# Kernel optimization log

Hardware: AMD Instinct MI355X
Metric: run time of the kernel (lower is better)

Reference implementation:

```python
import jax, jax.numpy as jnp
import numpy as np

DIM = 768
NUM_HEADS = 12
HEAD_DIM = DIM // NUM_HEADS


def setup_inputs() -> dict:
    key = jax.random.key(0)
    k1, k2, k3 = jax.random.split(key, 3)
    B, N, C = 1, 4096, DIM
    x = jax.random.normal(k1, (B, N, C), dtype=jnp.float32)
    w_qkv = jax.random.normal(k2, (C, 3 * C), dtype=jnp.float32) * (C ** -0.5)
    w_proj = jax.random.normal(k3, (C, C), dtype=jnp.float32) * (C ** -0.5)
    b_proj = jnp.zeros((C,), dtype=jnp.float32)
    return {"x": x, "w_qkv": w_qkv, "w_proj": w_proj, "b_proj": b_proj}


def reference(x, w_qkv, w_proj, b_proj):
    B, N, C = x.shape
    H, D = NUM_HEADS, HEAD_DIM
    scale = D ** -0.5
    # QKV projection (no bias), split into heads: [B, N, 3, H, D] -> bhnd
    qkv = (x @ w_qkv).reshape(B, N, 3, H, D)
    qkv = jnp.transpose(qkv, (2, 0, 3, 1, 4))  # [3, B, H, N, D]
    q, k, v = qkv[0], qkv[1], qkv[2]
    # world_size == 1 => all_gather is identity; full attention over N
    attn = jnp.einsum('bhnd,bhmd->bhnm', q * scale, k)
    attn = jax.nn.softmax(attn, axis=-1)
    out = jnp.einsum('bhnm,bhmd->bhnd', attn, v)
    out = jnp.transpose(out, (0, 2, 1, 3)).reshape(B, N, C)
    return out @ w_proj + b_proj
```

## Files before the change

kernel.cpp:

```cpp
#include <hip/hip_runtime.h>
#include <hip/hip_bf16.h>

#define NT 4096
#define CD 768
#define NH 12
#define HD 64
#define CQ 2304

typedef __bf16 bf;
typedef __bf16 v8bf __attribute__((ext_vector_type(8)));
typedef __bf16 v4bf __attribute__((ext_vector_type(4)));
typedef float  v4f  __attribute__((ext_vector_type(4)));

__device__ __forceinline__ void gld16(const bf* g, bf* l) {
  __builtin_amdgcn_global_load_lds(
      (__attribute__((address_space(1))) void*)g,
      (__attribute__((address_space(3))) void*)l,
      16, 0, 0);
}

__device__ __forceinline__ float fexp2(float x) {
#if defined(__HIP_DEVICE_COMPILE__)
  return __builtin_amdgcn_exp2f(x);
#else
  return x;
#endif
}

__global__ __launch_bounds__(256) void prep(
    const float* __restrict__ x, const float* __restrict__ wqkv,
    const float* __restrict__ wproj, bf* __restrict__ Xb,
    bf* __restrict__ WqkvT, bf* __restrict__ WpT) {
  __shared__ float tile[32][33];
  const int b = blockIdx.x, tid = threadIdx.x;
  if (b < 3072) {
    const int i = b * 256 + tid;
    const float4 v = ((const float4*)x)[i];
    bf o4[4] = {(bf)v.x, (bf)v.y, (bf)v.z, (bf)v.w};
    ((ushort4*)Xb)[i] = *(const ushort4*)o4;
    return;
  }
  const float* in;
  bf* out;
  int rows, cols, c0, r0;
  if (b < 4800) {
    const int t = b - 3072;
    in = wqkv; out = WqkvT; rows = CD; cols = CQ;
    c0 = (t % 72) * 32; r0 = (t / 72) * 32;
  } else {
    const int t = b - 4800;
    in = wproj; out = WpT; rows = CD; cols = CD;
    c0 = (t % 24) * 32; r0 = (t / 24) * 32;
  }
  const int tx = tid & 31, ty = tid >> 5;
#pragma unroll
  for (int j = 0; j < 32; j += 8)
    tile[ty + j][tx] = in[(size_t)(r0 + ty + j) * cols + (c0 + tx)];
  __syncthreads();
#pragma unroll
  for (int j = 0; j < 32; j += 8)
    out[(size_t)(c0 + ty + j) * rows + (r0 + tx)] = (bf)tile[tx][ty + j];
}

__global__ __launch_bounds__(256, 3) void gemm_qkv(
    const bf* __restrict__ A, const bf* __restrict__ Bt,
    bf* __restrict__ Qb, bf* __restrict__ Kb, bf* __restrict__ Vtb) {
  __shared__ __align__(16) bf As[128 * 64];
  __shared__ __align__(16) bf Bs[128 * 64];
  const int tid = threadIdx.x;
  const int lane = tid & 63, wave = tid >> 6;
  const int lane15 = lane & 15, quad = lane >> 4;
  const int waveM = wave & 1, waveN = wave >> 1;
  const int bm = blockIdx.x * 128;
  const int bn = blockIdx.y * 128;

  v4f acc[4][4];
#pragma unroll
  for (int i = 0; i < 4; ++i)
#pragma unroll
    for (int j = 0; j < 4; ++j) acc[i][j] = (v4f){0.f, 0.f, 0.f, 0.f};

  for (int k0 = 0; k0 < CD; k0 += 64) {
#pragma unroll
    for (int p = 0; p < 4; ++p) {
      const int t = tid + p * 256;
      const int r = t >> 3, u = t & 7;
      gld16(A + (size_t)(bm + r) * CD + k0 + ((u ^ (r & 7)) << 3), As + t * 8);
    }
#pragma unroll
    for (int p = 0; p < 4; ++p) {
      const int t = tid + p * 256;
      const int r = t >> 3, u = t & 7;
      gld16(Bt + (size_t)(bn + r) * CD + k0 + ((u ^ (r & 7)) << 3), Bs + t * 8);
    }
    asm volatile("s_waitcnt vmcnt(0)" ::: "memory");
    __syncthreads();

    v8bf af[4][2], bfr[4][2];
#pragma unroll
    for (int mt = 0; mt < 4; ++mt) {
      const int rr = waveM * 64 + mt * 16 + lane15;
      const int r7 = rr & 7;
      af[mt][0] = *(const v8bf*)(As + rr * 64 + ((quad ^ r7) << 3));
      af[mt][1] = *(const v8bf*)(As + rr * 64 + (((quad ^ 4) ^ r7) << 3));
    }
#pragma unroll
    for (int nt = 0; nt < 4; ++nt) {
      const int rr = waveN * 64 + nt * 16 + lane15;
      const int r7 = rr & 7;
      bfr[nt][0] = *(const v8bf*)(Bs + rr * 64 + ((quad ^ r7) << 3));
      bfr[nt][1] = *(const v8bf*)(Bs + rr * 64 + (((quad ^ 4) ^ r7) << 3));
    }
#pragma unroll
    for (int mt = 0; mt < 4; ++mt)
#pragma unroll
      for (int nt = 0; nt < 4; ++nt) {
        acc[mt][nt] = __builtin_amdgcn_mfma_f32_16x16x32_bf16(af[mt][0], bfr[nt][0], acc[mt][nt], 0, 0, 0);
        acc[mt][nt] = __builtin_amdgcn_mfma_f32_16x16x32_bf16(af[mt][1], bfr[nt][1], acc[mt][nt], 0, 0, 0);
      }
    __syncthreads();
  }

  const float QSCALE = 0.125f * 1.4426950408889634f;
#pragma unroll
  for (int mt = 0; mt < 4; ++mt) {
    const int rowB = bm + waveM * 64 + mt * 16 + quad * 4;
#pragma unroll
    for (int nt = 0; nt < 4; ++nt) {
      const int col = bn + waveN * 64 + nt * 16 + lane15;
      const int s = col / CD;
      const int rem = col - s * CD;
      const int h = rem >> 6, d = rem & 63;
      if (s == 2) {
        bf vp[4];
#pragma unroll
        for (int i = 0; i < 4; ++i) vp[i] = (bf)acc[mt][nt][i];
        const int pos = (rowB & ~31) + (((rowB & 15) >> 2) << 3) + (((rowB >> 4) & 1) << 2);
        *(uint2*)(Vtb + ((size_t)h * HD + d) * NT + pos) = *(const uint2*)vp;
      } else {
#pragma unroll
        for (int i = 0; i < 4; ++i) {
          const float v = acc[mt][nt][i];
          const int row = rowB + i;
          if (s == 0) Qb[((size_t)h * NT + row) * HD + d] = (bf)(v * QSCALE);
          else        Kb[((size_t)h * NT + row) * HD + d] = (bf)v;
        }
      }
    }
  }
}

__global__ __launch_bounds__(256, 4) void attn(
    const bf* __restrict__ Qb, const bf* __restrict__ Kb,
    const bf* __restrict__ Vtb, bf* __restrict__ Ob) {
  __shared__ __align__(16) char smem[32768];

  const int b = blockIdx.x;
  int h, qt;
  if (b < 512) { h = b & 7;        qt = b >> 3; }
  else { const int bb = b - 512; h = 8 + (bb & 3); qt = bb >> 2; }
  const int q0 = qt * 64;

  const int tid = threadIdx.x;
  const int wave = tid >> 6, lane = tid & 63;
  const int kh = wave & 1;
  const int sh = wave >> 1;
  const int lane15 = lane & 15, quad = lane >> 4;

  const bf* Kh = Kb + (size_t)h * NT * HD;
  const bf* Vh = Vtb + (size_t)h * HD * NT;

  v8bf aQ[2][2];
#pragma unroll
  for (int sl = 0; sl < 2; ++sl) {
    const int qrow = q0 + (sh * 2 + sl) * 16 + lane15;
    aQ[sl][0] = *(const v8bf*)(Qb + ((size_t)h * NT + qrow) * HD + quad * 8);
    aQ[sl][1] = *(const v8bf*)(Qb + ((size_t)h * NT + qrow) * HD + 32 + quad * 8);
  }

  v4f o[2][4];
#pragma unroll
  for (int sl = 0; sl < 2; ++sl)
#pragma unroll
    for (int dt = 0; dt < 4; ++dt) o[sl][dt] = (v4f){0.f, 0.f, 0.f, 0.f};
  float lsum[2] = {0.f, 0.f};

  auto stage = [&](int half, int kt) {
    bf* Kdst = (bf*)(smem + half * 16384);
    bf* Vdst = (bf*)(smem + half * 16384 + 8192);
#pragma unroll
    for (int p = 0; p < 2; ++p) {
      const int L = p * 256 + tid;
      const int r = L >> 3, u = L & 7;
      gld16(Kh + (size_t)(kt + r) * HD + ((u ^ (r & 7)) << 3), Kdst + L * 8);
    }
#pragma unroll
    for (int p = 0; p < 2; ++p) {
      const int L = p * 256 + tid;
      const int d = L >> 3, u = L & 7;
      gld16(Vh + (size_t)d * NT + kt + ((u ^ (d & 7)) << 3), Vdst + L * 8);
    }
  };

  stage(0, 0);
  asm volatile("s_waitcnt vmcnt(0)" ::: "memory");
  __syncthreads();

  for (int it = 0; it < NT / 64; ++it) {
    const int half = it & 1;
    if (it + 1 < NT / 64) stage(half ^ 1, (it + 1) * 64);

    const bf* Kbuf = (const bf*)(smem + half * 16384);
    const bf* Vbuf = (const bf*)(smem + half * 16384 + 8192);

    v4bf aPlo[2], aPhi[2];
#pragma unroll
    for (int e = 0; e < 2; ++e) {
      const int k = kh * 32 + e * 16 + lane15;
      const int k7 = k & 7;
      const v8bf bk0 = *(const v8bf*)(Kbuf + k * 64 + ((quad ^ k7) << 3));
      const v8bf bk1 = *(const v8bf*)(Kbuf + k * 64 + (((quad ^ 4) ^ k7) << 3));
#pragma unroll
      for (int sl = 0; sl < 2; ++sl) {
        v4f z = (v4f){0.f, 0.f, 0.f, 0.f};
        __builtin_amdgcn_s_setprio(1);
        z = __builtin_amdgcn_mfma_f32_16x16x32_bf16(bk0, aQ[sl][0], z, 0, 0, 0);
        z = __builtin_amdgcn_mfma_f32_16x16x32_bf16(bk1, aQ[sl][1], z, 0, 0, 0);
        __builtin_amdgcn_s_setprio(0);
        v4bf p4;
#pragma unroll
        for (int r = 0; r < 4; ++r) {
          const float p = fexp2(z[r]);
          lsum[sl] += p;
          p4[r] = (bf)p;
        }
        if (e == 0) aPlo[sl] = p4; else aPhi[sl] = p4;
      }
    }

#pragma unroll
    for (int dt = 0; dt < 4; ++dt) {
      const int d = dt * 16 + lane15;
      const v8bf bv = *(const v8bf*)(Vbuf + d * 64 + (((kh * 4 + quad) ^ (d & 7)) << 3));
      __builtin_amdgcn_s_setprio(1);
#pragma unroll
      for (int sl = 0; sl < 2; ++sl) {
        const v8bf aP8 = __builtin_shufflevector(aPlo[sl], aPhi[sl], 0, 1, 2, 3, 4, 5, 6, 7);
        o[sl][dt] = __builtin_amdgcn_mfma_f32_16x16x32_bf16(aP8, bv, o[sl][dt], 0, 0, 0);
      }
      __builtin_amdgcn_s_setprio(0);
    }

    asm volatile("s_waitcnt vmcnt(0)" ::: "memory");
    __syncthreads();
  }

#pragma unroll
  for (int sl = 0; sl < 2; ++sl) {
    lsum[sl] += __shfl_xor(lsum[sl], 16, 64);
    lsum[sl] += __shfl_xor(lsum[sl], 32, 64);
  }

  float* Red = (float*)smem;
  float* Ls  = (float*)(smem + 16384);
#pragma unroll
  for (int sl = 0; sl < 2; ++sl) {
    __syncthreads();
    float* reg = Red + wave * 1024;
#pragma unroll
    for (int dt = 0; dt < 4; ++dt)
      *(v4f*)(reg + dt * 256 + lane15 * 16 + quad * 4) = o[sl][dt];
    if (quad == 0) Ls[wave * 16 + lane15] = lsum[sl];
    __syncthreads();
    const int s = sh * 2 + sl;
    const float den = Ls[(sh * 2) * 16 + lane15] + Ls[(sh * 2 + 1) * 16 + lane15];
    const float linv = 1.f / den;
#pragma unroll
    for (int dh = 0; dh < 2; ++dh) {
      const int dt = kh * 2 + dh;
      v4f sum = *(const v4f*)(Red + (sh * 2) * 1024 + dt * 256 + lane15 * 16 + quad * 4);
      sum     += *(const v4f*)(Red + (sh * 2 + 1) * 1024 + dt * 256 + lane15 * 16 + quad * 4);
#pragma unroll
      for (int i = 0; i < 4; ++i) {
        const float linv_i = __shfl(linv, quad * 4 + i, 64);
        const int row = q0 + s * 16 + quad * 4 + i;
        Ob[(size_t)row * CD + h * HD + dt * 16 + lane15] = (bf)(sum[i] * linv_i);
      }
    }
  }
}

__global__ __launch_bounds__(256, 4) void gemm_proj(
    const bf* __restrict__ A, const bf* __restrict__ Bt,
    const float* __restrict__ bias, float* __restrict__ out) {
  __shared__ __align__(16) bf As[2][64 * 32];
  __shared__ __align__(16) bf Bs[2][128 * 32];
  const int tid = threadIdx.x;
  const int lane = tid & 63, wave = tid >> 6;
  const int lane15 = lane & 15, quad = lane >> 4;
  const int bm = blockIdx.x * 64;
  const int bn = blockIdx.y * 128;

  v4f acc[4][2];
#pragma unroll
  for (int i = 0; i < 4; ++i)
#pragma unroll
    for (int j = 0; j < 2; ++j) acc[i][j] = (v4f){0.f, 0.f, 0.f, 0.f};

  auto stageG = [&](int half, int k0) {
    {
      const int r = tid >> 2, c = (tid & 3) * 8;
      gld16(A + (size_t)(bm + r) * CD + k0 + c, As[half] + tid * 8);
    }
#pragma unroll
    for (int p = 0; p < 2; ++p) {
      const int t = tid + p * 256;
      const int r = t >> 2, c = (t & 3) * 8;
      gld16(Bt + (size_t)(bn + r) * CD + k0 + c, Bs[half] + t * 8);
    }
  };

  stageG(0, 0);
  asm volatile("s_waitcnt vmcnt(0)" ::: "memory");
  __syncthreads();

  for (int it = 0; it < CD / 32; ++it) {
    const int half = it & 1;
    if (it + 1 < CD / 32) stageG(half ^ 1, (it + 1) * 32);

    v8bf af[4], bfr[2];
#pragma unroll
    for (int mt = 0; mt < 4; ++mt)
      af[mt] = *(const v8bf*)(As[half] + (mt * 16 + lane15) * 32 + quad * 8);
#pragma unroll
    for (int nt = 0; nt < 2; ++nt)
      bfr[nt] = *(const v8bf*)(Bs[half] + (wave * 32 + nt * 16 + lane15) * 32 + quad * 8);
#pragma unroll
    for (int mt = 0; mt < 4; ++mt)
#pragma unroll
      for (int nt = 0; nt < 2; ++nt)
        acc[mt][nt] = __builtin_amdgcn_mfma_f32_16x16x32_bf16(af[mt], bfr[nt], acc[mt][nt], 0, 0, 0);

    asm volatile("s_waitcnt vmcnt(0)" ::: "memory");
    __syncthreads();
  }

#pragma unroll
  for (int mt = 0; mt < 4; ++mt) {
    const int rowB = bm + mt * 16 + quad * 4;
#pragma unroll
    for (int nt = 0; nt < 2; ++nt) {
      const int col = bn + wave * 32 + nt * 16 + lane15;
      const float bcol = bias[col];
#pragma unroll
      for (int i = 0; i < 4; ++i)
        out[(size_t)(rowB + i) * CD + col] = acc[mt][nt][i] + bcol;
    }
  }
}

extern "C" void kernel_launch(void* const* d_in, const int* in_sizes, int n_in,
                              void* d_out, int out_size, void* d_ws, size_t ws_size,
                              hipStream_t stream) {
  const float* x     = (const float*)d_in[0];
  const float* wqkv  = (const float*)d_in[1];
  const float* wproj = (const float*)d_in[2];
  const float* bproj = (const float*)d_in[3];
  float* out = (float*)d_out;

  bf* ws    = (bf*)d_ws;
  bf* Xb    = ws;  ws += (size_t)NT * CD;
  bf* WqkvT = ws;  ws += (size_t)CQ * CD;
  bf* WpT   = ws;  ws += (size_t)CD * CD;
  bf* Qb    = ws;  ws += (size_t)NH * NT * HD;
  bf* Kb    = ws;  ws += (size_t)NH * NT * HD;
  bf* Vtb   = ws;  ws += (size_t)NH * NT * HD;
  bf* Ob    = ws;  ws += (size_t)NT * CD;

  prep<<<5376, 256, 0, stream>>>(x, wqkv, wproj, Xb, WqkvT, WpT);
  gemm_qkv<<<dim3(NT / 128, CQ / 128), 256, 0, stream>>>(Xb, WqkvT, Qb, Kb, Vtb);
  attn<<<768, 256, 0, stream>>>(Qb, Kb, Vtb, Ob);
  gemm_proj<<<dim3(NT / 64, CD / 128), 256, 0, stream>>>(Ob, WpT, bproj, out);
}
```

Measured before the change: 171.0 us.

## Triple-buffer K/V staging and compute softmax denominator with MFMA

Moves the attention K/V staging from a double buffer with a full vmcnt(0) wait plus syncthreads per tile to a triple-buffered ring. It prefetches two tiles ahead and waits with vmcnt(4) and a bare s_barrier, so global loads overlap more compute. The row-sum of probabilities now comes from an extra MFMA against a vector of ones instead of scalar adds and cross-lane shuffles, which cuts VALU work. Shared memory grows to 48KB, which may lower occupancy, and the row sum now uses bf16-rounded probabilities.

```diff
diff --git a/kernel.cpp b/kernel.cpp
--- a/kernel.cpp
+++ b/kernel.cpp
@@ -153,7 +153,7 @@
 __global__ __launch_bounds__(256, 4) void attn(
     const bf* __restrict__ Qb, const bf* __restrict__ Kb,
     const bf* __restrict__ Vtb, bf* __restrict__ Ob) {
-  __shared__ __align__(16) char smem[32768];
+  __shared__ __align__(16) char smem[49152];
 
   const int b = blockIdx.x;
   int h, qt;
@@ -183,11 +183,14 @@
   for (int sl = 0; sl < 2; ++sl)
 #pragma unroll
     for (int dt = 0; dt < 4; ++dt) o[sl][dt] = (v4f){0.f, 0.f, 0.f, 0.f};
-  float lsum[2] = {0.f, 0.f};
-
-  auto stage = [&](int half, int kt) {
-    bf* Kdst = (bf*)(smem + half * 16384);
-    bf* Vdst = (bf*)(smem + half * 16384 + 8192);
+  v4f den[2] = {(v4f){0.f, 0.f, 0.f, 0.f}, (v4f){0.f, 0.f, 0.f, 0.f}};
+  v8bf vone;
+#pragma unroll
+  for (int i = 0; i < 8; ++i) vone[i] = (bf)1.0f;
+
+  auto stage = [&](int buf, int kt) {
+    bf* Kdst = (bf*)(smem + buf * 16384);
+    bf* Vdst = (bf*)(smem + buf * 16384 + 8192);
 #pragma unroll
     for (int p = 0; p < 2; ++p) {
       const int L = p * 256 + tid;
@@ -202,16 +205,9 @@
     }
   };
 
-  stage(0, 0);
-  asm volatile("s_waitcnt vmcnt(0)" ::: "memory");
-  __syncthreads();
-
-  for (int it = 0; it < NT / 64; ++it) {
-    const int half = it & 1;
-    if (it + 1 < NT / 64) stage(half ^ 1, (it + 1) * 64);
-
-    const bf* Kbuf = (const bf*)(smem + half * 16384);
-    const bf* Vbuf = (const bf*)(smem + half * 16384 + 8192);
+  auto compute = [&](int buf) {
+    const bf* Kbuf = (const bf*)(smem + buf * 16384);
+    const bf* Vbuf = (const bf*)(smem + buf * 16384 + 8192);
 
     v4bf aPlo[2], aPhi[2];
 #pragma unroll
@@ -229,37 +225,49 @@
         __builtin_amdgcn_s_setprio(0);
         v4bf p4;
 #pragma unroll
-        for (int r = 0; r < 4; ++r) {
-          const float p = fexp2(z[r]);
-          lsum[sl] += p;
-          p4[r] = (bf)p;
-        }
+        for (int r = 0; r < 4; ++r) p4[r] = (bf)fexp2(z[r]);
         if (e == 0) aPlo[sl] = p4; else aPhi[sl] = p4;
       }
     }
 
+    v8bf aP8[2];
+#pragma unroll
+    for (int sl = 0; sl < 2; ++sl) {
+      aP8[sl] = __builtin_shufflevector(aPlo[sl], aPhi[sl], 0, 1, 2, 3, 4, 5, 6, 7);
+      den[sl] = __builtin_amdgcn_mfma_f32_16x16x32_bf16(aP8[sl], vone, den[sl], 0, 0, 0);
+    }
 #pragma unroll
     for (int dt = 0; dt < 4; ++dt) {
       const int d = dt * 16 + lane15;
       const v8bf bv = *(const v8bf*)(Vbuf + d * 64 + (((kh * 4 + quad) ^ (d & 7)) << 3));
       __builtin_amdgcn_s_setprio(1);
 #pragma unroll
-      for (int sl = 0; sl < 2; ++sl) {
-        const v8bf aP8 = __builtin_shufflevector(aPlo[sl], aPhi[sl], 0, 1, 2, 3, 4, 5, 6, 7);
-        o[sl][dt] = __builtin_amdgcn_mfma_f32_16x16x32_bf16(aP8, bv, o[sl][dt], 0, 0, 0);
-      }
+      for (int sl = 0; sl < 2; ++sl)
+        o[sl][dt] = __builtin_amdgcn_mfma_f32_16x16x32_bf16(aP8[sl], bv, o[sl][dt], 0, 0, 0);
       __builtin_amdgcn_s_setprio(0);
     }
-
-    asm volatile("s_waitcnt vmcnt(0)" ::: "memory");
-    __syncthreads();
-  }
-
-#pragma unroll
-  for (int sl = 0; sl < 2; ++sl) {
-    lsum[sl] += __shfl_xor(lsum[sl], 16, 64);
-    lsum[sl] += __shfl_xor(lsum[sl], 32, 64);
-  }
+  };
+
+  stage(0, 0);
+  stage(1, 64);
+
+#pragma unroll 1
+  for (int grp = 0; grp < 21; ++grp) {
+    const int it0 = grp * 3;
+#pragma unroll
+    for (int j = 0; j < 3; ++j) {
+      const int it = it0 + j;
+      asm volatile("s_waitcnt vmcnt(4)" ::: "memory");
+      __builtin_amdgcn_s_barrier();
+      asm volatile("" ::: "memory");
+      if (it + 2 < 64) stage((it + 2) % 3, (it + 2) * 64);
+      compute(it % 3);
+    }
+  }
+  asm volatile("s_waitcnt vmcnt(0)" ::: "memory");
+  __builtin_amdgcn_s_barrier();
+  asm volatile("" ::: "memory");
+  compute(0);
 
   float* Red = (float*)smem;
   float* Ls  = (float*)(smem + 16384);
@@ -270,11 +278,14 @@
 #pragma unroll
     for (int dt = 0; dt < 4; ++dt)
       *(v4f*)(reg + dt * 256 + lane15 * 16 + quad * 4) = o[sl][dt];
-    if (quad == 0) Ls[wave * 16 + lane15] = lsum[sl];
+    if (lane15 == 0) {
+#pragma unroll
+      for (int i = 0; i < 4; ++i) Ls[wave * 16 + quad * 4 + i] = den[sl][i];
+    }
     __syncthreads();
     const int s = sh * 2 + sl;
-    const float den = Ls[(sh * 2) * 16 + lane15] + Ls[(sh * 2 + 1) * 16 + lane15];
-    const float linv = 1.f / den;
+    const float dsum = Ls[(sh * 2) * 16 + lane15] + Ls[(sh * 2 + 1) * 16 + lane15];
+    const float linv = 1.f / dsum;
 #pragma unroll
     for (int dh = 0; dh < 2; ++dh) {
       const int dt = kh * 2 + dh;
```

Measured after the change: 173.7 us. About the same (+1.6%).
